# Kernel optimization log

Hardware: AMD Instinct MI355X
Metric: run time of the kernel (lower is better)

The kernel has to match this reference:

```python
import jax, jax.numpy as jnp
import numpy as np
from jax import lax

B, T, H, M, K, Q, P = 32, 128, 256, 1000, 3, 4, 2  # batch, phones, hidden, max_mel_len, kernel, q_out, p_out


def _ln(x, g, b, eps=1e-5):
    mu = jnp.mean(x, -1, keepdims=True)
    var = jnp.mean((x - mu) ** 2, -1, keepdims=True)
    return (x - mu) * lax.rsqrt(var + eps) * g + b


def _forward(x, x_mask, x_dur, params):
    (proj_w, proj_b, conv_w, conv_b, conv_g, conv_beta,
     q_w1, q_b1, q_g, q_beta, q_w2, q_b2,
     p_w1, p_b1, p_g, p_beta, p_w2, p_b2,
     proj1_w, proj1_b, proj2_w, proj2_b, projo_w, projo_b) = params

    valid = (~x_mask).astype(x.dtype)[:, :, None]                      # (B,T,1), 1 = real phone
    # proj -> ConvBlock (shared between the w and c branches; dropout is identity in eval)
    h = x @ proj_w + proj_b                                            # (B,T,H)
    hc = lax.conv_general_dilated((h * valid).transpose(0, 2, 1), conv_w,
                                  (1,), 'SAME',
                                  dimension_numbers=('NCH', 'OIH', 'NCH'))
    hc = hc.transpose(0, 2, 1) + conv_b                                # (B,T,8)
    hc = jax.nn.silu(_ln(hc, conv_g, conv_beta)) * valid               # (B,T,8)

    mel_lens = jnp.minimum(jnp.round(jnp.sum(x_dur, -1)).astype(jnp.int32), M)
    mel_pad = jnp.arange(M)[None, :] >= mel_lens[:, None]              # (B,M) True = padded frame
    mask = x_mask[:, None, :] | mel_pad[:, :, None]                    # (B,M,T)

    e = jnp.cumsum(x_dur, -1)                                          # phone end times
    s = e - x_dur                                                      # phone start times
    t = jnp.arange(1, M + 1, dtype=x.dtype)
    E = jnp.where(mask, 0.0, e[:, None, :] - t[None, :, None])         # (B,M,T)
    S = jnp.where(mask, 0.0, t[None, :, None] - s[:, None, :])         # (B,M,T)

    feat = jnp.concatenate([jnp.broadcast_to(hc[:, None], (B, M, T, 8)),
                            S[..., None], E[..., None]], axis=-1)      # (B,M,T,10)

    # mlp_q scores -> masked softmax over phone axis
    sc = jax.nn.silu(_ln(feat @ q_w1 + q_b1, q_g, q_beta)) @ q_w2 + q_b2   # (B,M,T,Q)
    sc = jnp.where(x_mask[:, None, :, None], -jnp.inf, sc)
    w = jax.nn.softmax(sc, axis=2)
    w = jnp.where(mel_pad[:, :, None, None], 0.0, w)                   # (B,M,T,Q)

    # mlp_p per-(frame,phone) auxiliary features
    c = jax.nn.silu(_ln(feat @ p_w1 + p_b1, p_g, p_beta)) @ p_w2 + p_b2    # (B,M,T,P)

    # dual einsum combine (matches torch permute+view ordering: q-major then feature)
    wh = jnp.einsum('bmnq,bnh->bmqh', w, x).reshape(B, M, Q * H) @ proj1_w + proj1_b
    wc = jnp.einsum('bmnq,bmnp->bmqp', w, c).reshape(B, M, Q * P) @ proj2_w + proj2_b
    o = jnp.where(mel_pad[:, :, None], 0.0, wh + wc) @ projo_w + projo_b   # (B,M,2H)

    mel_mask = jnp.broadcast_to(mel_pad[:, :, None], (B, M, T))
    return o, mel_mask, mel_lens, jnp.transpose(w, (0, 3, 1, 2))


def setup_inputs() -> dict:
    key = jax.random.key(0)
    ks = jax.random.split(key, 16)
    x = jax.random.normal(ks[0], (B, T, H), jnp.float32)
    x_lengths = jax.random.randint(ks[1], (B,), T // 2, T + 1).at[0].set(T)
    x_mask = jnp.arange(T)[None, :] >= x_lengths[:, None]              # True = pad
    x_dur = jax.random.uniform(ks[2], (B, T), jnp.float32, 2.0, 10.0)
    x_dur = x_dur * (~x_mask)
    x_dur = x_dur.at[0].multiply(2.0)  # element 0 total duration > M -> static max_mel_len = M

    def xavier(k, shape):
        return jax.random.normal(k, shape, jnp.float32) * jnp.sqrt(2.0 / (shape[0] + shape[1]))

    return dict(
        x=x, x_mask=x_mask, x_dur=x_dur, x_lengths=x_lengths,
        proj_w=xavier(ks[3], (H, H)), proj_b=jnp.zeros((H,)),
        conv_w=jax.random.normal(ks[4], (8, H, K), jnp.float32) * 0.05, conv_b=jnp.zeros((8,)),
        conv_g=jnp.ones((8,)), conv_beta=jnp.zeros((8,)),
        q_w1=xavier(ks[5], (10, Q)), q_b1=jnp.zeros((Q,)),
        q_g=jnp.ones((Q,)), q_beta=jnp.zeros((Q,)),
        q_w2=xavier(ks[6], (Q, Q)), q_b2=jnp.zeros((Q,)),
        p_w1=xavier(ks[7], (10, P)), p_b1=jnp.zeros((P,)),
        p_g=jnp.ones((P,)), p_beta=jnp.zeros((P,)),
        p_w2=xavier(ks[8], (P, P)), p_b2=jnp.zeros((P,)),
        proj1_w=xavier(ks[9], (H * Q, H)), proj1_b=jnp.zeros((H,)),
        proj2_w=xavier(ks[10], (Q * P, H)), proj2_b=jnp.zeros((H,)),
        projo_w=xavier(ks[11], (H, 2 * H)), projo_b=jnp.zeros((2 * H,)),
    )


def reference(x, x_mask, x_dur, x_lengths,
              proj_w, proj_b, conv_w, conv_b, conv_g, conv_beta,
              q_w1, q_b1, q_g, q_beta, q_w2, q_b2,
              p_w1, p_b1, p_g, p_beta, p_w2, p_b2,
              proj1_w, proj1_b, proj2_w, proj2_b, projo_w, projo_b):
    params = (proj_w, proj_b, conv_w, conv_b, conv_g, conv_beta,
              q_w1, q_b1, q_g, q_beta, q_w2, q_b2,
              p_w1, p_b1, p_g, p_beta, p_w2, p_b2,
              proj1_w, proj1_b, proj2_w, proj2_b, projo_w, projo_b)
    return _forward(x, x_mask, x_dur, params)
```

## Files before the change

### kernel.cpp

```cpp
#include <hip/hip_runtime.h>
#include <math.h>

#define BB 32
#define TT 128
#define HH 256
#define MM 1000

typedef __attribute__((ext_vector_type(8))) short short8;
typedef __attribute__((ext_vector_type(4))) float floatx4;

__device__ inline void fma4(float4& a, const float4 b, float s) {
    a.x += b.x * s; a.y += b.y * s; a.z += b.z * s; a.w += b.w * s;
}

__device__ inline unsigned short f2bf(float f) {
    union { float f; unsigned int u; } c; c.f = f;
    unsigned int u = c.u;
    return (unsigned short)((u + 0x7FFFu + ((u >> 16) & 1u)) >> 16);
}

__device__ inline float bf2f(unsigned short h) {
    union { unsigned int u; float f; } c; c.u = ((unsigned int)h) << 16; return c.f;
}


__global__ __launch_bounds__(256) void kF1(
    const float* __restrict__ x, const float* __restrict__ pw_h_,
    const float* __restrict__ pb_h, float* __restrict__ h,
    const float* __restrict__ p1w, const float* __restrict__ po,
    float* __restrict__ PWpart,
    unsigned short* __restrict__ xh, unsigned short* __restrict__ xl,
    const float* __restrict__ dur, float* __restrict__ e_cum,
    int* __restrict__ ml_i, float* __restrict__ ml_out,
    unsigned short* __restrict__ w_bf) {
    __shared__ __align__(16) float S1[4096];
    int gb = blockIdx.x;
    int tid = threadIdx.x;

    if (gb < 256) {
        float (*xs)[HH] = (float(*)[HH])S1;
        int b = gb >> 3, tt = gb & 7;
        int t0 = tt * 16;
        for (int e = tid; e < 16 * HH; e += 256) {
            int r = e >> 8, i = e & 255;
            xs[r][i] = x[(b * TT + t0 + r) * HH + i];
        }
        __syncthreads();
        int jg = tid & 63, rg = tid >> 6;
        int j4 = jg * 4;
        float4 bias = *(const float4*)(pb_h + j4);
        float4 acc[4];
        #pragma unroll
        for (int ri = 0; ri < 4; ++ri) acc[ri] = bias;
        #pragma unroll 4
        for (int i = 0; i < HH; ++i) {
            float4 wv = *(const float4*)(pw_h_ + i * HH + j4);
            #pragma unroll
            for (int ri = 0; ri < 4; ++ri) fma4(acc[ri], wv, xs[rg * 4 + ri][i]);
        }
        #pragma unroll
        for (int ri = 0; ri < 4; ++ri)
            *(float4*)(h + (b * TT + t0 + rg * 4 + ri) * HH + j4) = acc[ri];
    } else if (gb < 768) {
        float (*S)[64] = (float(*)[64])S1;
        int blk = gb - 256;
        int ks = blk & 3, colT = (blk >> 2) & 7, ht = blk >> 5;
        int q = colT >> 1, j0 = (colT & 1) * 256;
        int h0 = ht * 16, k0 = ks * 64;
        for (int e = tid; e < 1024; e += 256) {
            int r = e >> 6, c = e & 63;
            S[r][c] = p1w[(q * 256 + h0 + r) * 256 + k0 + c];
        }
        __syncthreads();
        int jg = tid & 63, rg = tid >> 6;
        int jcol = j0 + jg * 4;
        float4 acc[4];
        #pragma unroll
        for (int r = 0; r < 4; ++r) acc[r] = make_float4(0, 0, 0, 0);
        float4 nb = *(const float4*)(po + (size_t)k0 * 512 + jcol);
        for (int c = 0; c < 64; ++c) {
            float4 cur = nb;
            if (c < 63) nb = *(const float4*)(po + (size_t)(k0 + c + 1) * 512 + jcol);
            #pragma unroll
            for (int r = 0; r < 4; ++r) fma4(acc[r], cur, S[rg * 4 + r][c]);
        }
        #pragma unroll
        for (int r = 0; r < 4; ++r) {
            int hh = h0 + rg * 4 + r;
            *(float4*)(PWpart + (size_t)ks * 524288 + hh * 2048 + q * 512 + jcol) = acc[r];
        }
    } else if (gb < 1792) {
        int idx = ((gb - 768) * 256 + tid) * 4;
        float4 v = *(const float4*)(x + idx);
        float vv[4] = {v.x, v.y, v.z, v.w};
        union { unsigned short us[4]; uint2 u; } hi, lo;
        #pragma unroll
        for (int k = 0; k < 4; ++k) {
            unsigned short hv = f2bf(vv[k]);
            hi.us[k] = hv;
            lo.us[k] = f2bf(vv[k] - bf2f(hv));
        }
        *(uint2*)(xh + idx) = hi.u;
        *(uint2*)(xl + idx) = lo.u;
    } else {
        int b = gb - 1792;
        if (tid < 64) {
            #pragma unroll
            for (int q = 0; q < 4; ++q) {
                uint4* dst = (uint4*)(w_bf + (((size_t)(b * 4 + q)) * 1024 + 1000) * 128);
                for (int e = tid; e < 384; e += 64) dst[e] = make_uint4(0, 0, 0, 0);
            }
            if (tid == 0) {
                float run = 0.f;
                const float* d = dur + b * TT;
                float* e = e_cum + b * TT;
                for (int t = 0; t < TT; ++t) { run += d[t]; e[t] = run; }
                int ml = (int)rintf(run);
                if (ml > MM) ml = MM;
                if (ml < 0) ml = 0;
                ml_i[b] = ml;
                ml_out[b] = (float)ml;
            }
        }
    }
}

__global__ __launch_bounds__(256) void kF2(
    const float* __restrict__ h, const float* __restrict__ cw,
    const int* __restrict__ xlen,
    const float* __restrict__ PWpart,
    unsigned short* __restrict__ pwh, unsigned short* __restrict__ pwl,
    const float* __restrict__ p2w, const float* __restrict__ po,
    const float* __restrict__ p1b, const float* __restrict__ p2b,
    const float* __restrict__ pob,
    float* __restrict__ P2o, float* __restrict__ bvec,
    const float* __restrict__ cb, const float* __restrict__ cg,
    const float* __restrict__ cbeta,
    const float* __restrict__ qw1, const float* __restrict__ qb1,
    const float* __restrict__ pw1, const float* __restrict__ pb1,
    const float* __restrict__ e_cum, const float* __restrict__ dur,
    float* __restrict__ baseq, float* __restrict__ basep) {
    __shared__ __align__(16) float S2[10906];
    int gb = blockIdx.x;
    int tid = threadIdx.x;

    if (gb < 256) {
        float (*hs)[257] = (float(*)[257])S2;
        float (*cws)[769] = (float(*)[769])(S2 + 4626);
        float (*hc)[8] = (float(*)[8])(S2 + 10778);
        int b = gb >> 3, tt = gb & 7;
        int t0 = tt * 16;
        int L = xlen[b];
        for (int e = tid; e < 18 * 256; e += 256) {
            int r = e >> 8, i = e & 255;
            int t = t0 - 1 + r;
            float v = 0.f;
            if (t >= 0 && t < TT && t < L) v = h[((size_t)b * TT + t) * HH + i];
            hs[r][i] = v;
        }
        for (int e = tid; e < 6144; e += 256) {
            int o = e / 768, rem = e - o * 768;
            cws[o][rem] = cw[e];
        }
        __syncthreads();
        if (tid < 128) {
            int o = tid >> 4, tl = tid & 15;
            float acc = 0.f;
            #pragma unroll
            for (int k = 0; k < 3; ++k) {
                const float* wr = &cws[o][k];
                const float* hr = hs[tl + k];
                #pragma unroll 8
                for (int i = 0; i < 256; ++i) acc += hr[i] * wr[i * 3];
            }
            hc[tl][o] = acc;
        }
        __syncthreads();
        if (tid < 16) {
            int t = t0 + tid;
            float v[8];
            float mu = 0.f;
            #pragma unroll
            for (int o = 0; o < 8; ++o) { v[o] = hc[tid][o] + cb[o]; mu += v[o]; }
            mu *= 0.125f;
            float var = 0.f;
            #pragma unroll
            for (int o = 0; o < 8; ++o) { float d = v[o] - mu; var += d * d; }
            var *= 0.125f;
            float rs = 1.0f / sqrtf(var + 1e-5f);
            float valid = (t < L) ? 1.f : 0.f;
            #pragma unroll
            for (int o = 0; o < 8; ++o) {
                float a = (v[o] - mu) * rs * cg[o] + cbeta[o];
                v[o] = a / (1.f + expf(-a)) * valid;
            }
            float e = e_cum[b * TT + t];
            float s_ = e - dur[b * TT + t];
            #pragma unroll
            for (int j = 0; j < 4; ++j) {
                float acc = qb1[j];
                #pragma unroll
                for (int o = 0; o < 8; ++o) acc += v[o] * qw1[o * 4 + j];
                acc += e * qw1[9 * 4 + j] - s_ * qw1[8 * 4 + j];
                baseq[(b * TT + t) * 4 + j] = acc;
            }
            #pragma unroll
            for (int j = 0; j < 2; ++j) {
                float acc = pb1[j];
                #pragma unroll
                for (int o = 0; o < 8; ++o) acc += v[o] * pw1[o * 2 + j];
                acc += e * pw1[9 * 2 + j] - s_ * pw1[8 * 2 + j];
                basep[(b * TT + t) * 2 + j] = acc;
            }
        }
    } else if (gb < 384) {
        float (*S)[65] = (float(*)[65])S2;
        int blk = gb - 256;
        int nt = blk & 31, ct = blk >> 5;
        int c0 = ct * 64, n0 = nt * 64;
        for (int e = tid; e < 4096; e += 256) {
            int cc = e >> 6, nn = e & 63;
            size_t off = (size_t)(c0 + cc) * 2048 + n0 + nn;
            float v = PWpart[off] + PWpart[524288 + off]
                    + PWpart[2 * 524288 + off] + PWpart[3 * 524288 + off];
            S[cc][nn] = v;
        }
        __syncthreads();
        for (int e = tid; e < 4096; e += 256) {
            int nn = e >> 6, cc = e & 63;
            float v = S[cc][nn];
            unsigned short hv = f2bf(v);
            size_t d = (size_t)(n0 + nn) * 256 + c0 + cc;
            pwh[d] = hv;
            pwl[d] = f2bf(v - bf2f(hv));
        }
    } else {
        for (int j = tid; j < 512; j += 256) {
            float acc[9];
            #pragma unroll
            for (int r = 0; r < 9; ++r) acc[r] = 0.f;
            for (int c = 0; c < HH; ++c) {
                float pv = po[c * 512 + j];
                #pragma unroll
                for (int r = 0; r < 8; ++r) acc[r] += p2w[r * HH + c] * pv;
                acc[8] += (p1b[c] + p2b[c]) * pv;
            }
            #pragma unroll
            for (int r = 0; r < 8; ++r) P2o[r * 512 + j] = acc[r];
            bvec[j] = acc[8] + pob[j];
        }
    }
}

__device__ inline int swzk(int row, int chunk) {
    return row * 32 + ((chunk ^ ((row >> 1) & 3)) << 3);
}

__global__ __launch_bounds__(256) void kF3(
    const unsigned short* __restrict__ xh, const unsigned short* __restrict__ xl,
    const unsigned short* __restrict__ pwh, const unsigned short* __restrict__ pwl,
    unsigned short* __restrict__ A2T,
    const float* __restrict__ baseq, const float* __restrict__ basep,
    const float* __restrict__ qw1, const float* __restrict__ qg,
    const float* __restrict__ qbeta, const float* __restrict__ qw2,
    const float* __restrict__ qb2,
    const float* __restrict__ pw1, const float* __restrict__ pg,
    const float* __restrict__ pbeta, const float* __restrict__ pw2,
    const float* __restrict__ pb2,
    const int* __restrict__ xlen, const int* __restrict__ ml_i,
    float* __restrict__ w_out, float* __restrict__ mm_out,
    float* __restrict__ wc8, unsigned short* __restrict__ w_bf) {
    __shared__ __align__(16) unsigned short SM[16384];
    int gblk = blockIdx.x;
    int tid = threadIdx.x;

    if (gblk >= 512) {
        int blk = gblk - 512;
        int b = blk / 250;
        int mg = blk - b * 250;
        int wv = tid >> 6, lane = tid & 63;
        int m = mg * 4 + wv;
        int ml = ml_i[b];
        int t1 = lane, t2 = lane + 64;
        bool pad = (m >= ml);
        size_t mmbase = ((size_t)b * MM + m) * TT;
        mm_out[mmbase + t1] = pad ? 1.f : 0.f;
        mm_out[mmbase + t2] = pad ? 1.f : 0.f;
        if (pad) {
            #pragma unroll
            for (int q = 0; q < 4; ++q) {
                size_t wb = ((size_t)(b * 4 + q) * MM + m) * TT;
                w_out[wb + t1] = 0.f;
                w_out[wb + t2] = 0.f;
                unsigned short* wbq = w_bf + (((size_t)(b * 4 + q)) * 1024 + m) * 128;
                wbq[t1] = 0; wbq[t2] = 0;
            }
            if (lane == 0) {
                #pragma unroll
                for (int r = 0; r < 8; ++r) wc8[((size_t)b * MM + m) * 8 + r] = 0.f;
            }
            return;
        }
        int L = xlen[b];
        float mp1 = (float)(m + 1);
        float dq[4];
        #pragma unroll
        for (int j = 0; j < 4; ++j) dq[j] = mp1 * (qw1[8 * 4 + j] - qw1[9 * 4 + j]);

        float sc1[4], sc2[4];
        float c1v[2], c2v[2];
        #pragma unroll
        for (int half = 0; half < 2; ++half) {
            int t = half ? t2 : t1;
            float* sc = half ? sc2 : sc1;
            float* cv = half ? c2v : c1v;
            if (t < L) {
                float4 bq = *(const float4*)(baseq + ((size_t)b * TT + t) * 4);
                float z[4] = {bq.x + dq[0], bq.y + dq[1], bq.z + dq[2], bq.w + dq[3]};
                float mu = 0.25f * (z[0] + z[1] + z[2] + z[3]);
                float var = 0.f;
                #pragma unroll
                for (int j = 0; j < 4; ++j) { float d = z[j] - mu; var += d * d; }
                var *= 0.25f;
                float rs = 1.f / sqrtf(var + 1e-5f);
                float a[4];
                #pragma unroll
                for (int j = 0; j < 4; ++j) {
                    float av = (z[j] - mu) * rs * qg[j] + qbeta[j];
                    a[j] = av / (1.f + expf(-av));
                }
                #pragma unroll
                for (int q = 0; q < 4; ++q) {
                    float s = qb2[q];
                    #pragma unroll
                    for (int j = 0; j < 4; ++j) s += a[j] * qw2[j * 4 + q];
                    sc[q] = s;
                }
                float z0 = basep[((size_t)b * TT + t) * 2 + 0] + mp1 * (pw1[16] - pw1[18]);
                float z1 = basep[((size_t)b * TT + t) * 2 + 1] + mp1 * (pw1[17] - pw1[19]);
                float pmu = 0.5f * (z0 + z1);
                float d0 = z0 - pmu, d1 = z1 - pmu;
                float pvar = 0.5f * (d0 * d0 + d1 * d1);
                float prs = 1.f / sqrtf(pvar + 1e-5f);
                float a0 = d0 * prs * pg[0] + pbeta[0];
                float a1 = d1 * prs * pg[1] + pbeta[1];
                a0 = a0 / (1.f + expf(-a0));
                a1 = a1 / (1.f + expf(-a1));
                cv[0] = pb2[0] + a0 * pw2[0] + a1 * pw2[2];
                cv[1] = pb2[1] + a0 * pw2[1] + a1 * pw2[3];
            } else {
                sc[0] = sc[1] = sc[2] = sc[3] = -__builtin_inff();
                cv[0] = cv[1] = 0.f;
            }
        }
        float w1[4], w2[4];
        #pragma unroll
        for (int q = 0; q < 4; ++q) {
            float mx = fmaxf(sc1[q], sc2[q]);
            #pragma unroll
            for (int off = 32; off > 0; off >>= 1) mx = fmaxf(mx, __shfl_xor(mx, off, 64));
            float e1 = expf(sc1[q] - mx);
            float e2 = expf(sc2[q] - mx);
            float s = e1 + e2;
            #pragma unroll
            for (int off = 32; off > 0; off >>= 1) s += __shfl_xor(s, off, 64);
            w1[q] = e1 / s;
            w2[q] = e2 / s;
            size_t wb = ((size_t)(b * 4 + q) * MM + m) * TT;
            w_out[wb + t1] = w1[q];
            w_out[wb + t2] = w2[q];
            unsigned short* wbq = w_bf + (((size_t)(b * 4 + q)) * 1024 + m) * 128;
            wbq[t1] = f2bf(w1[q]);
            wbq[t2] = f2bf(w2[q]);
        }
        float red[8];
        #pragma unroll
        for (int r8 = 0; r8 < 8; ++r8) {
            int q = r8 >> 1, p = r8 & 1;
            float v = w1[q] * c1v[p] + w2[q] * c2v[p];
            #pragma unroll
            for (int off = 32; off > 0; off >>= 1) v += __shfl_xor(v, off, 64);
            red[r8] = v;
        }
        if (lane == 0) {
            #pragma unroll
            for (int r8 = 0; r8 < 8; ++r8) wc8[((size_t)b * MM + m) * 8 + r8] = red[r8];
        }
        return;
    }

    unsigned short* Ah = SM;
    unsigned short* Al = SM + 4096;
    unsigned short* Bh = SM + 8192;
    unsigned short* Bl = SM + 12288;
    int blk = gblk;
    int b = blk >> 4, nt = blk & 15;
    int n0 = nt * 128;
    int lane = tid & 63, wv = tid >> 6;
    int wm = wv & 1, wn = wv >> 1;

    floatx4 acc[16];
    #pragma unroll
    for (int i = 0; i < 16; ++i) acc[i] = (floatx4){0.f, 0.f, 0.f, 0.f};

    int srow = tid >> 1, shalf = tid & 1;
    const unsigned short* gxh = xh + ((size_t)(b * TT + srow) * 256 + shalf * 16);
    const unsigned short* gxl = xl + ((size_t)(b * TT + srow) * 256 + shalf * 16);
    const unsigned short* gph = pwh + ((size_t)(n0 + srow) * 256 + shalf * 16);
    const unsigned short* gpl = pwl + ((size_t)(n0 + srow) * 256 + shalf * 16);
    int wAd0 = swzk(srow, 2 * shalf);
    int wAd1 = swzk(srow, 2 * shalf + 1);

    int ra = wm * 64 + (lane & 15);
    int rb = wn * 64 + (lane & 15);
    int cq = lane >> 4;

    for (int kc = 0; kc < 256; kc += 32) {
        uint4 a0 = *(const uint4*)(gxh + kc);
        uint4 a1 = *(const uint4*)(gxh + kc + 8);
        uint4 a2 = *(const uint4*)(gxl + kc);
        uint4 a3 = *(const uint4*)(gxl + kc + 8);
        uint4 b0 = *(const uint4*)(gph + kc);
        uint4 b1 = *(const uint4*)(gph + kc + 8);
        uint4 b2 = *(const uint4*)(gpl + kc);
        uint4 b3 = *(const uint4*)(gpl + kc + 8);
        *(uint4*)&Ah[wAd0] = a0; *(uint4*)&Ah[wAd1] = a1;
        *(uint4*)&Al[wAd0] = a2; *(uint4*)&Al[wAd1] = a3;
        *(uint4*)&Bh[wAd0] = b0; *(uint4*)&Bh[wAd1] = b1;
        *(uint4*)&Bl[wAd0] = b2; *(uint4*)&Bl[wAd1] = b3;
        __syncthreads();
        short8 afh[4], afl[4], bfh[4], bfl[4];
        #pragma unroll
        for (int i = 0; i < 4; ++i) {
            afh[i] = *(const short8*)&Ah[swzk(ra + i * 16, cq)];
            afl[i] = *(const short8*)&Al[swzk(ra + i * 16, cq)];
            bfh[i] = *(const short8*)&Bh[swzk(rb + i * 16, cq)];
            bfl[i] = *(const short8*)&Bl[swzk(rb + i * 16, cq)];
        }
        #pragma unroll
        for (int i = 0; i < 4; ++i)
            #pragma unroll
            for (int j = 0; j < 4; ++j) {
                floatx4 c = acc[i * 4 + j];
                c = __builtin_amdgcn_mfma_f32_16x16x32_bf16(afh[i], bfh[j], c, 0, 0, 0);
                c = __builtin_amdgcn_mfma_f32_16x16x32_bf16(afh[i], bfl[j], c, 0, 0, 0);
                c = __builtin_amdgcn_mfma_f32_16x16x32_bf16(afl[i], bfh[j], c, 0, 0, 0);
                acc[i * 4 + j] = c;
            }
        __syncthreads();
    }

    unsigned short* OT = SM;
    #pragma unroll
    for (int i = 0; i < 4; ++i)
        #pragma unroll
        for (int j = 0; j < 4; ++j) {
            int nloc = wn * 64 + j * 16 + (lane & 15);
            int tb = wm * 64 + i * 16 + ((lane >> 4) << 2);
            union { unsigned short us[4]; uint2 v; } pk;
            #pragma unroll
            for (int r = 0; r < 4; ++r) pk.us[r] = f2bf(acc[i * 4 + j][r]);
            int chunk = tb >> 3, sub = tb & 7;
            *(uint2*)&OT[nloc * 128 + (((chunk ^ (nloc & 15)) << 3) | sub)] = pk.v;
        }
    __syncthreads();
    int q = n0 >> 9, jb = n0 & 511;
    for (int u = tid; u < 2048; u += 256) {
        int nrow = u >> 4, seg = u & 15;
        uint4 v = *(const uint4*)&OT[nrow * 128 + ((seg ^ (nrow & 15)) << 3)];
        *(uint4*)(A2T + (((size_t)(b * 4 + q) * 512) + jb + nrow) * 128 + seg * 8) = v;
    }
}

__global__ __launch_bounds__(256, 2) void k_main(
    const unsigned short* __restrict__ w_bf, const unsigned short* __restrict__ A2T,
    const float* __restrict__ wc8, const float* __restrict__ P2o,
    const float* __restrict__ bvec, const float* __restrict__ pob,
    const int* __restrict__ ml_i, float* __restrict__ o_out) {
    __shared__ __align__(16) unsigned short Asm[2][128 * 40];
    __shared__ __align__(16) unsigned short Bsm[2][128 * 40];
    int wgid = blockIdx.x;
    int blk = (wgid & 7) * 128 + (wgid >> 3);
    int nt = blk & 3, mt = (blk >> 2) & 7, b = blk >> 5;
    int m0 = mt * 128, n0 = nt * 128;
    int tid = threadIdx.x;
    int ml = ml_i[b];

    if (m0 >= ml) {
        float* pb_s = (float*)&Asm[0][0];
        if (tid < 128) pb_s[tid] = pob[n0 + tid];
        __syncthreads();
        int col4 = (tid & 31) * 4;
        float4 pv = *(const float4*)&pb_s[col4];
        for (int r = tid >> 5; r < 128; r += 8) {
            int m = m0 + r;
            if (m < MM)
                *(float4*)(o_out + ((size_t)b * MM + m) * 512 + n0 + col4) = pv;
        }
        return;
    }

    int lane = tid & 63, wv = tid >> 6;
    int wm = wv & 1, wn = wv >> 1;

    floatx4 acc[16];
    #pragma unroll
    for (int i = 0; i < 16; ++i) acc[i] = (floatx4){0.f, 0.f, 0.f, 0.f};

    int rl = lane >> 4;
    int cl = lane & 15;
    int ra = wm * 64 + cl;
    int rb = wn * 64 + cl;

    int srow = tid >> 2, schunk = tid & 3;
    int doff = srow * 40 + schunk * 8;
    const size_t bq4 = (size_t)b * 4;

    #pragma unroll
    for (int j = 0; j < 2; ++j) {
        int row = srow + j * 64;
        uint4 va = *(const uint4*)(w_bf + ((bq4 + 0) * 1024 + m0 + row) * 128 + schunk * 8);
        uint4 vb = *(const uint4*)(A2T + ((bq4 + 0) * 512 + n0 + row) * 128 + schunk * 8);
        *(uint4*)&Asm[0][doff + j * 2560] = va;
        *(uint4*)&Bsm[0][doff + j * 2560] = vb;
    }
    __syncthreads();

    int cur = 0;
    for (int s = 0; s < 16; ++s) {
        uint4 la[2], lb[2];
        if (s < 15) {
            int q = (s + 1) >> 2, koff = ((s + 1) & 3) * 32;
            #pragma unroll
            for (int j = 0; j < 2; ++j) {
                int row = srow + j * 64;
                la[j] = *(const uint4*)(w_bf +
                    ((bq4 + q) * 1024 + m0 + row) * 128 + koff + schunk * 8);
                lb[j] = *(const uint4*)(A2T +
                    ((bq4 + q) * 512 + n0 + row) * 128 + koff + schunk * 8);
            }
        }
        {
            int co = rl * 8;
            short8 af[4], bfr[4];
            #pragma unroll
            for (int i = 0; i < 4; ++i)
                af[i] = *(const short8*)&Asm[cur][(ra + i * 16) * 40 + co];
            #pragma unroll
            for (int j2 = 0; j2 < 4; ++j2)
                bfr[j2] = *(const short8*)&Bsm[cur][(rb + j2 * 16) * 40 + co];
            #pragma unroll
            for (int i = 0; i < 4; ++i)
                #pragma unroll
                for (int j2 = 0; j2 < 4; ++j2)
                    acc[i * 4 + j2] = __builtin_amdgcn_mfma_f32_16x16x32_bf16(
                        af[i], bfr[j2], acc[i * 4 + j2], 0, 0, 0);
        }
        if (s < 15) {
            #pragma unroll
            for (int j = 0; j < 2; ++j) {
                *(uint4*)&Asm[cur ^ 1][doff + j * 2560] = la[j];
                *(uint4*)&Bsm[cur ^ 1][doff + j * 2560] = lb[j];
            }
        }
        __syncthreads();
        cur ^= 1;
    }

    float* wc8s = (float*)&Asm[0][0];
    float* P2os = (float*)&Bsm[0][0];
    float* bvs  = (float*)&Bsm[0][0] + 1024;
    float* pobs = (float*)&Bsm[0][0] + 1152;
    for (int e = tid; e < 1024; e += 256) {
        int mm_ = e >> 3, r = e & 7;
        int m = m0 + mm_;
        wc8s[e] = (m < MM) ? wc8[((size_t)b * MM + m) * 8 + r] : 0.f;
    }
    for (int e = tid; e < 1024; e += 256) {
        int r = e >> 7, j = e & 127;
        P2os[e] = P2o[r * 512 + n0 + j];
    }
    if (tid < 128) {
        bvs[tid] = bvec[n0 + tid];
        pobs[tid] = pob[n0 + tid];
    }
    __syncthreads();
    #pragma unroll
    for (int i = 0; i < 4; ++i) {
        #pragma unroll
        for (int j = 0; j < 4; ++j) {
            int nloc = wn * 64 + j * 16 + (lane & 15);
            #pragma unroll
            for (int reg = 0; reg < 4; ++reg) {
                int mloc = wm * 64 + i * 16 + (lane >> 4) * 4 + reg;
                int m = m0 + mloc;
                if (m >= MM) continue;
                float v;
                if (m < ml) {
                    v = acc[i * 4 + j][reg] + bvs[nloc];
                    #pragma unroll
                    for (int r8 = 0; r8 < 8; ++r8)
                        v += wc8s[mloc * 8 + r8] * P2os[r8 * 128 + nloc];
                } else {
                    v = pobs[nloc];
                }
                o_out[((size_t)b * MM + m) * 512 + n0 + nloc] = v;
            }
        }
    }
}

extern "C" void kernel_launch(void* const* d_in, const int* in_sizes, int n_in,
                              void* d_out, int out_size, void* d_ws, size_t ws_size,
                              hipStream_t stream) {
    (void)in_sizes; (void)n_in; (void)out_size; (void)ws_size;
    const float* x      = (const float*)d_in[0];
    const float* dur    = (const float*)d_in[2];
    const int*   xlen   = (const int*)d_in[3];
    const float* proj_w = (const float*)d_in[4];
    const float* proj_b = (const float*)d_in[5];
    const float* conv_w = (const float*)d_in[6];
    const float* conv_b = (const float*)d_in[7];
    const float* conv_g = (const float*)d_in[8];
    const float* conv_be= (const float*)d_in[9];
    const float* q_w1   = (const float*)d_in[10];
    const float* q_b1   = (const float*)d_in[11];
    const float* q_g    = (const float*)d_in[12];
    const float* q_be   = (const float*)d_in[13];
    const float* q_w2   = (const float*)d_in[14];
    const float* q_b2   = (const float*)d_in[15];
    const float* p_w1   = (const float*)d_in[16];
    const float* p_b1   = (const float*)d_in[17];
    const float* p_g    = (const float*)d_in[18];
    const float* p_be   = (const float*)d_in[19];
    const float* p_w2   = (const float*)d_in[20];
    const float* p_b2   = (const float*)d_in[21];
    const float* p1w    = (const float*)d_in[22];
    const float* p1b    = (const float*)d_in[23];
    const float* p2w    = (const float*)d_in[24];
    const float* p2b    = (const float*)d_in[25];
    const float* pow_   = (const float*)d_in[26];
    const float* pob    = (const float*)d_in[27];

    float* ws    = (float*)d_ws;
    float* e_cum = ws + 0;
    float* baseq = ws + 36864;
    float* basep = ws + 53248;
    float* h     = ws + 61440;
    unsigned short* pw_h = (unsigned short*)(ws + 1110016);
    unsigned short* pw_l = (unsigned short*)(ws + 1372160);
    unsigned short* A2T = (unsigned short*)(ws + 1634304);
    float* wc8   = ws + 5828608;
    float* P2o   = ws + 6084608;
    float* bvec  = ws + 6088704;
    int*   ml_i  = (int*)(ws + 6089216);
    float* PWpart= ws + 6090752;
    unsigned short* w_bf = (unsigned short*)(ws + 8187904);
    unsigned short* x_hi = (unsigned short*)(ws + 16576512);
    unsigned short* x_lo = (unsigned short*)(ws + 17100800);

    float* o_out  = (float*)d_out;
    float* mm_out = o_out + 16384000;
    float* ml_out = o_out + 20480000;
    float* w_out  = o_out + 20480032;

    kF1<<<dim3(1824), dim3(256), 0, stream>>>(x, proj_w, proj_b, h,
                                              p1w, pow_, PWpart,
                                              x_hi, x_lo,
                                              dur, e_cum, ml_i, ml_out, w_bf);
    kF2<<<dim3(385), dim3(256), 0, stream>>>(h, conv_w, xlen,
                                             PWpart, pw_h, pw_l,
                                             p2w, pow_, p1b, p2b, pob, P2o, bvec,
                                             conv_b, conv_g, conv_be,
                                             q_w1, q_b1, p_w1, p_b1,
                                             e_cum, dur, baseq, basep);
    kF3<<<dim3(8512), dim3(256), 0, stream>>>(x_hi, x_lo, pw_h, pw_l, A2T,
                                              baseq, basep,
                                              q_w1, q_g, q_be, q_w2, q_b2,
                                              p_w1, p_g, p_be, p_w2, p_b2,
                                              xlen, ml_i, w_out, mm_out, wc8, w_bf);
    k_main<<<dim3(BB * 32), dim3(256), 0, stream>>>(w_bf, A2T, wc8, P2o, bvec,
                                                    pob, ml_i, o_out);
}
```

Measured before the change: 372.8 us.

## Load GEMM A-fragments directly from global, write A2T without LDS staging

In the kF3 GEMM path, the A operand (x hi/lo) fragments are now read straight from global memory per wave instead of being staged through shared memory. LDS use drops to the B tiles only, which halves the shared allocation. The transposed output is written to A2T directly from registers as 8-byte stores, removing the LDS transpose and its extra barrier, at the cost of less coalesced global writes and redundant A reads across waves. k_main's launch bounds are also raised to ask for three blocks per SM, which may force fewer registers per thread and cause spills.

```diff
diff --git a/kernel.cpp b/kernel.cpp
--- a/kernel.cpp
+++ b/kernel.cpp
@@ -270,7 +270,7 @@
     const int* __restrict__ xlen, const int* __restrict__ ml_i,
     float* __restrict__ w_out, float* __restrict__ mm_out,
     float* __restrict__ wc8, unsigned short* __restrict__ w_bf) {
-    __shared__ __align__(16) unsigned short SM[16384];
+    __shared__ __align__(16) unsigned short SM[8192];
     int gblk = blockIdx.x;
     int tid = threadIdx.x;
 
@@ -389,10 +389,8 @@
         return;
     }
 
-    unsigned short* Ah = SM;
-    unsigned short* Al = SM + 4096;
-    unsigned short* Bh = SM + 8192;
-    unsigned short* Bl = SM + 12288;
+    unsigned short* Bh = SM;
+    unsigned short* Bl = SM + 4096;
     int blk = gblk;
     int b = blk >> 4, nt = blk & 15;
     int n0 = nt * 128;
@@ -404,8 +402,6 @@
     for (int i = 0; i < 16; ++i) acc[i] = (floatx4){0.f, 0.f, 0.f, 0.f};
 
     int srow = tid >> 1, shalf = tid & 1;
-    const unsigned short* gxh = xh + ((size_t)(b * TT + srow) * 256 + shalf * 16);
-    const unsigned short* gxl = xl + ((size_t)(b * TT + srow) * 256 + shalf * 16);
     const unsigned short* gph = pwh + ((size_t)(n0 + srow) * 256 + shalf * 16);
     const unsigned short* gpl = pwl + ((size_t)(n0 + srow) * 256 + shalf * 16);
     int wAd0 = swzk(srow, 2 * shalf);
@@ -414,26 +410,26 @@
     int ra = wm * 64 + (lane & 15);
     int rb = wn * 64 + (lane & 15);
     int cq = lane >> 4;
+    const unsigned short* axh = xh + ((size_t)(b * TT) + 0) * 256 + cq * 8;
+    const unsigned short* axl = xl + ((size_t)(b * TT) + 0) * 256 + cq * 8;
 
     for (int kc = 0; kc < 256; kc += 32) {
-        uint4 a0 = *(const uint4*)(gxh + kc);
-        uint4 a1 = *(const uint4*)(gxh + kc + 8);
-        uint4 a2 = *(const uint4*)(gxl + kc);
-        uint4 a3 = *(const uint4*)(gxl + kc + 8);
         uint4 b0 = *(const uint4*)(gph + kc);
         uint4 b1 = *(const uint4*)(gph + kc + 8);
         uint4 b2 = *(const uint4*)(gpl + kc);
         uint4 b3 = *(const uint4*)(gpl + kc + 8);
-        *(uint4*)&Ah[wAd0] = a0; *(uint4*)&Ah[wAd1] = a1;
-        *(uint4*)&Al[wAd0] = a2; *(uint4*)&Al[wAd1] = a3;
         *(uint4*)&Bh[wAd0] = b0; *(uint4*)&Bh[wAd1] = b1;
         *(uint4*)&Bl[wAd0] = b2; *(uint4*)&Bl[wAd1] = b3;
-        __syncthreads();
-        short8 afh[4], afl[4], bfh[4], bfl[4];
+        short8 afh[4], afl[4];
         #pragma unroll
         for (int i = 0; i < 4; ++i) {
-            afh[i] = *(const short8*)&Ah[swzk(ra + i * 16, cq)];
-            afl[i] = *(const short8*)&Al[swzk(ra + i * 16, cq)];
+            afh[i] = *(const short8*)(axh + (size_t)(ra + i * 16) * 256 + kc);
+            afl[i] = *(const short8*)(axl + (size_t)(ra + i * 16) * 256 + kc);
+        }
+        __syncthreads();
+        short8 bfh[4], bfl[4];
+        #pragma unroll
+        for (int i = 0; i < 4; ++i) {
             bfh[i] = *(const short8*)&Bh[swzk(rb + i * 16, cq)];
             bfl[i] = *(const short8*)&Bl[swzk(rb + i * 16, cq)];
         }
@@ -450,7 +446,7 @@
         __syncthreads();
     }
 
-    unsigned short* OT = SM;
+    int q = n0 >> 9, jb = n0 & 511;
     #pragma unroll
     for (int i = 0; i < 4; ++i)
         #pragma unroll
@@ -460,19 +456,11 @@
             union { unsigned short us[4]; uint2 v; } pk;
             #pragma unroll
             for (int r = 0; r < 4; ++r) pk.us[r] = f2bf(acc[i * 4 + j][r]);
-            int chunk = tb >> 3, sub = tb & 7;
-            *(uint2*)&OT[nloc * 128 + (((chunk ^ (nloc & 15)) << 3) | sub)] = pk.v;
-        }
-    __syncthreads();
-    int q = n0 >> 9, jb = n0 & 511;
-    for (int u = tid; u < 2048; u += 256) {
-        int nrow = u >> 4, seg = u & 15;
-        uint4 v = *(const uint4*)&OT[nrow * 128 + ((seg ^ (nrow & 15)) << 3)];
-        *(uint4*)(A2T + (((size_t)(b * 4 + q) * 512) + jb + nrow) * 128 + seg * 8) = v;
-    }
-}
-
-__global__ __launch_bounds__(256, 2) void k_main(
+            *(uint2*)(A2T + (((size_t)(b * 4 + q) * 512) + jb + nloc) * 128 + tb) = pk.v;
+        }
+}
+
+__global__ __launch_bounds__(256, 3) void k_main(
     const unsigned short* __restrict__ w_bf, const unsigned short* __restrict__ A2T,
     const float* __restrict__ wc8, const float* __restrict__ P2o,
     const float* __restrict__ bvec, const float* __restrict__ pob,
```

After: 383.5 us. 1.03x slower.

## Widen k_main N-tile to 256 and fuse x bf16 split into proj blocks

Applied to the files above, without the earlier changes.

The main MFMA GEMM kernel now computes 128x256 output tiles per workgroup instead of 128x128. This halves the grid, reuses each A tile across twice as many columns, and doubles the accumulator count per thread. Separately, the hi/lo bf16 split of x is folded into the projection blocks of kF1, which already stage x rows in shared memory, so the dedicated conversion blocks and their extra global read of x are dropped. The wider tile raises register and LDS pressure, which may lower occupancy under launch_bounds(256,2), and the smaller grid may leave compute units underused.

```diff
diff --git a/kernel.cpp b/kernel.cpp
--- a/kernel.cpp
+++ b/kernel.cpp
@@ -46,6 +46,22 @@
             xs[r][i] = x[(b * TT + t0 + r) * HH + i];
         }
         __syncthreads();
+        {
+            int r = tid >> 4, i0 = (tid & 15) * 16;
+            union { unsigned short us[16]; uint4 v[2]; } He, Lo;
+            #pragma unroll
+            for (int k = 0; k < 16; ++k) {
+                float xv = xs[r][i0 + k];
+                unsigned short hv = f2bf(xv);
+                He.us[k] = hv;
+                Lo.us[k] = f2bf(xv - bf2f(hv));
+            }
+            size_t off = ((size_t)(b * TT + t0 + r)) * 256 + i0;
+            *(uint4*)(xh + off) = He.v[0];
+            *(uint4*)(xh + off + 8) = He.v[1];
+            *(uint4*)(xl + off) = Lo.v[0];
+            *(uint4*)(xl + off + 8) = Lo.v[1];
+        }
         int jg = tid & 63, rg = tid >> 6;
         int j4 = jg * 4;
         float4 bias = *(const float4*)(pb_h + j4);
@@ -89,21 +105,8 @@
             int hh = h0 + rg * 4 + r;
             *(float4*)(PWpart + (size_t)ks * 524288 + hh * 2048 + q * 512 + jcol) = acc[r];
         }
-    } else if (gb < 1792) {
-        int idx = ((gb - 768) * 256 + tid) * 4;
-        float4 v = *(const float4*)(x + idx);
-        float vv[4] = {v.x, v.y, v.z, v.w};
-        union { unsigned short us[4]; uint2 u; } hi, lo;
-        #pragma unroll
-        for (int k = 0; k < 4; ++k) {
-            unsigned short hv = f2bf(vv[k]);
-            hi.us[k] = hv;
-            lo.us[k] = f2bf(vv[k] - bf2f(hv));
-        }
-        *(uint2*)(xh + idx) = hi.u;
-        *(uint2*)(xl + idx) = lo.u;
     } else {
-        int b = gb - 1792;
+        int b = gb - 768;
         if (tid < 64) {
             #pragma unroll
             for (int q = 0; q < 4; ++q) {
@@ -478,21 +481,21 @@
     const float* __restrict__ bvec, const float* __restrict__ pob,
     const int* __restrict__ ml_i, float* __restrict__ o_out) {
     __shared__ __align__(16) unsigned short Asm[2][128 * 40];
-    __shared__ __align__(16) unsigned short Bsm[2][128 * 40];
+    __shared__ __align__(16) unsigned short Bsm[2][256 * 40];
     int wgid = blockIdx.x;
-    int blk = (wgid & 7) * 128 + (wgid >> 3);
-    int nt = blk & 3, mt = (blk >> 2) & 7, b = blk >> 5;
-    int m0 = mt * 128, n0 = nt * 128;
+    int blk = (wgid & 7) * 64 + (wgid >> 3);
+    int nt = blk & 1, mt = (blk >> 1) & 7, b = blk >> 4;
+    int m0 = mt * 128, n0 = nt * 256;
     int tid = threadIdx.x;
     int ml = ml_i[b];
 
     if (m0 >= ml) {
         float* pb_s = (float*)&Asm[0][0];
-        if (tid < 128) pb_s[tid] = pob[n0 + tid];
-        __syncthreads();
-        int col4 = (tid & 31) * 4;
+        pb_s[tid] = pob[n0 + tid];
+        __syncthreads();
+        int col4 = (tid & 63) * 4;
         float4 pv = *(const float4*)&pb_s[col4];
-        for (int r = tid >> 5; r < 128; r += 8) {
+        for (int r = tid >> 6; r < 128; r += 4) {
             int m = m0 + r;
             if (m < MM)
                 *(float4*)(o_out + ((size_t)b * MM + m) * 512 + n0 + col4) = pv;
@@ -503,14 +506,14 @@
     int lane = tid & 63, wv = tid >> 6;
     int wm = wv & 1, wn = wv >> 1;
 
-    floatx4 acc[16];
+    floatx4 acc[32];
     #pragma unroll
-    for (int i = 0; i < 16; ++i) acc[i] = (floatx4){0.f, 0.f, 0.f, 0.f};
+    for (int i = 0; i < 32; ++i) acc[i] = (floatx4){0.f, 0.f, 0.f, 0.f};
 
     int rl = lane >> 4;
     int cl = lane & 15;
     int ra = wm * 64 + cl;
-    int rb = wn * 64 + cl;
+    int rb = wn * 128 + cl;
 
     int srow = tid >> 2, schunk = tid & 3;
     int doff = srow * 40 + schunk * 8;
@@ -520,15 +523,19 @@
     for (int j = 0; j < 2; ++j) {
         int row = srow + j * 64;
         uint4 va = *(const uint4*)(w_bf + ((bq4 + 0) * 1024 + m0 + row) * 128 + schunk * 8);
+        *(uint4*)&Asm[0][doff + j * 2560] = va;
+    }
+    #pragma unroll
+    for (int j = 0; j < 4; ++j) {
+        int row = srow + j * 64;
         uint4 vb = *(const uint4*)(A2T + ((bq4 + 0) * 512 + n0 + row) * 128 + schunk * 8);
-        *(uint4*)&Asm[0][doff + j * 2560] = va;
         *(uint4*)&Bsm[0][doff + j * 2560] = vb;
     }
     __syncthreads();
 
     int cur = 0;
     for (int s = 0; s < 16; ++s) {
-        uint4 la[2], lb[2];
+        uint4 la[2], lb[4];
         if (s < 15) {
             int q = (s + 1) >> 2, koff = ((s + 1) & 3) * 32;
             #pragma unroll
@@ -536,32 +543,37 @@
                 int row = srow + j * 64;
                 la[j] = *(const uint4*)(w_bf +
                     ((bq4 + q) * 1024 + m0 + row) * 128 + koff + schunk * 8);
+            }
+            #pragma unroll
+            for (int j = 0; j < 4; ++j) {
+                int row = srow + j * 64;
                 lb[j] = *(const uint4*)(A2T +
                     ((bq4 + q) * 512 + n0 + row) * 128 + koff + schunk * 8);
             }
         }
         {
             int co = rl * 8;
-            short8 af[4], bfr[4];
+            short8 af[4], bfr[8];
             #pragma unroll
             for (int i = 0; i < 4; ++i)
                 af[i] = *(const short8*)&Asm[cur][(ra + i * 16) * 40 + co];
             #pragma unroll
-            for (int j2 = 0; j2 < 4; ++j2)
+            for (int j2 = 0; j2 < 8; ++j2)
                 bfr[j2] = *(const short8*)&Bsm[cur][(rb + j2 * 16) * 40 + co];
             #pragma unroll
             for (int i = 0; i < 4; ++i)
                 #pragma unroll
-                for (int j2 = 0; j2 < 4; ++j2)
-                    acc[i * 4 + j2] = __builtin_amdgcn_mfma_f32_16x16x32_bf16(
-                        af[i], bfr[j2], acc[i * 4 + j2], 0, 0, 0);
+                for (int j2 = 0; j2 < 8; ++j2)
+                    acc[i * 8 + j2] = __builtin_amdgcn_mfma_f32_16x16x32_bf16(
+                        af[i], bfr[j2], acc[i * 8 + j2], 0, 0, 0);
         }
         if (s < 15) {
             #pragma unroll
-            for (int j = 0; j < 2; ++j) {
+            for (int j = 0; j < 2; ++j)
                 *(uint4*)&Asm[cur ^ 1][doff + j * 2560] = la[j];
+            #pragma unroll
+            for (int j = 0; j < 4; ++j)
                 *(uint4*)&Bsm[cur ^ 1][doff + j * 2560] = lb[j];
-            }
         }
         __syncthreads();
         cur ^= 1;
@@ -569,27 +581,25 @@
 
     float* wc8s = (float*)&Asm[0][0];
     float* P2os = (float*)&Bsm[0][0];
-    float* bvs  = (float*)&Bsm[0][0] + 1024;
-    float* pobs = (float*)&Bsm[0][0] + 1152;
+    float* bvs  = (float*)&Bsm[0][0] + 2048;
+    float* pobs = (float*)&Bsm[0][0] + 2304;
     for (int e = tid; e < 1024; e += 256) {
         int mm_ = e >> 3, r = e & 7;
         int m = m0 + mm_;
         wc8s[e] = (m < MM) ? wc8[((size_t)b * MM + m) * 8 + r] : 0.f;
     }
-    for (int e = tid; e < 1024; e += 256) {
-        int r = e >> 7, j = e & 127;
-        P2os[e] = P2o[r * 512 + n0 + j];
-    }
-    if (tid < 128) {
-        bvs[tid] = bvec[n0 + tid];
-        pobs[tid] = pob[n0 + tid];
-    }
+    for (int e = tid; e < 2048; e += 256) {
+        int r = e >> 8, jj = e & 255;
+        P2os[e] = P2o[r * 512 + n0 + jj];
+    }
+    bvs[tid] = bvec[n0 + tid];
+    pobs[tid] = pob[n0 + tid];
     __syncthreads();
     #pragma unroll
     for (int i = 0; i < 4; ++i) {
         #pragma unroll
-        for (int j = 0; j < 4; ++j) {
-            int nloc = wn * 64 + j * 16 + (lane & 15);
+        for (int j = 0; j < 8; ++j) {
+            int nloc = wn * 128 + j * 16 + (lane & 15);
             #pragma unroll
             for (int reg = 0; reg < 4; ++reg) {
                 int mloc = wm * 64 + i * 16 + (lane >> 4) * 4 + reg;
@@ -597,10 +607,10 @@
                 if (m >= MM) continue;
                 float v;
                 if (m < ml) {
-                    v = acc[i * 4 + j][reg] + bvs[nloc];
+                    v = acc[i * 8 + j][reg] + bvs[nloc];
                     #pragma unroll
                     for (int r8 = 0; r8 < 8; ++r8)
-                        v += wc8s[mloc * 8 + r8] * P2os[r8 * 128 + nloc];
+                        v += wc8s[mloc * 8 + r8] * P2os[r8 * 256 + nloc];
                 } else {
                     v = pobs[nloc];
                 }
@@ -664,10 +674,10 @@
     float* ml_out = o_out + 20480000;
     float* w_out  = o_out + 20480032;
 
-    kF1<<<dim3(1824), dim3(256), 0, stream>>>(x, proj_w, proj_b, h,
-                                              p1w, pow_, PWpart,
-                                              x_hi, x_lo,
-                                              dur, e_cum, ml_i, ml_out, w_bf);
+    kF1<<<dim3(800), dim3(256), 0, stream>>>(x, proj_w, proj_b, h,
+                                             p1w, pow_, PWpart,
+                                             x_hi, x_lo,
+                                             dur, e_cum, ml_i, ml_out, w_bf);
     kF2<<<dim3(385), dim3(256), 0, stream>>>(h, conv_w, xlen,
                                              PWpart, pw_h, pw_l,
                                              p2w, pow_, p1b, p2b, pob, P2o, bvec,
@@ -679,6 +689,6 @@
                                               q_w1, q_g, q_be, q_w2, q_b2,
                                               p_w1, p_g, p_be, p_w2, p_b2,
                                               xlen, ml_i, w_out, mm_out, wc8, w_bf);
-    k_main<<<dim3(BB * 32), dim3(256), 0, stream>>>(w_bf, A2T, wc8, P2o, bvec,
-                                                    pob, ml_i, o_out);
-}
+    k_main<<<dim3(512), dim3(256), 0, stream>>>(w_bf, A2T, wc8, P2o, bvec,
+                                                pob, ml_i, o_out);
+}
```

Result: no change. 380.2 us (+2.0%).
